# Optimization experiments

Hardware: AMD Instinct MI355X
Metric: run time of the kernel (lower is better)

Reference implementation:

```python
import jax, jax.numpy as jnp
import numpy as np
import math

N = 40000
E = 1280000
HID = 128
NF = 128
NG = 50
L = 3
CUTOFF = 10.0


def ssp(x):
    # shifted softplus: softplus(x) - log(2)
    return jax.nn.softplus(x) - jnp.float32(math.log(2.0))


def setup_inputs() -> dict:
    key = jax.random.key(0)
    ks = jax.random.split(key, 16)
    z = jax.random.randint(ks[0], (N,), 0, 100)
    pos = jax.random.normal(ks[1], (N, 3), dtype=jnp.float32) * 3.0
    batch = jnp.zeros((N,), dtype=jnp.int32)
    edge_index = jax.random.randint(ks[2], (2, E), 0, N)
    s = 0.1
    emb = jax.random.normal(ks[3], (100, HID), dtype=jnp.float32) * s
    mlp_w1 = jax.random.normal(ks[4], (L, NG, NF), dtype=jnp.float32) * s
    mlp_b1 = jnp.zeros((L, NF), dtype=jnp.float32)
    mlp_w2 = jax.random.normal(ks[5], (L, NF, NF), dtype=jnp.float32) * s
    mlp_b2 = jnp.zeros((L, NF), dtype=jnp.float32)
    conv_w1 = jax.random.normal(ks[6], (L, HID, NF), dtype=jnp.float32) * s  # no bias
    conv_w2 = jax.random.normal(ks[7], (L, NF, HID), dtype=jnp.float32) * s
    conv_b2 = jnp.zeros((L, HID), dtype=jnp.float32)
    lin_w = jax.random.normal(ks[8], (L, HID, HID), dtype=jnp.float32) * s
    lin_b = jnp.zeros((L, HID), dtype=jnp.float32)
    lin1_w = jax.random.normal(ks[9], (HID, HID // 2), dtype=jnp.float32) * s
    lin1_b = jnp.zeros((HID // 2,), dtype=jnp.float32)
    return {
        "z": z, "pos": pos, "batch": batch, "edge_index": edge_index,
        "emb": emb, "mlp_w1": mlp_w1, "mlp_b1": mlp_b1, "mlp_w2": mlp_w2,
        "mlp_b2": mlp_b2, "conv_w1": conv_w1, "conv_w2": conv_w2,
        "conv_b2": conv_b2, "lin_w": lin_w, "lin_b": lin_b,
        "lin1_w": lin1_w, "lin1_b": lin1_b,
    }


def reference(z, pos, batch, edge_index, emb, mlp_w1, mlp_b1, mlp_w2, mlp_b2,
              conv_w1, conv_w2, conv_b2, lin_w, lin_b, lin1_w, lin1_b):
    n = z.shape[0]
    row, col = edge_index[0], edge_index[1]
    # edge distances (radius-graph edge weights)
    diff = pos[row] - pos[col]                       # [E,3]
    edge_weight = jnp.sqrt(jnp.sum(diff * diff, axis=-1))  # [E]
    # Gaussian smearing
    offset = jnp.linspace(0.0, CUTOFF, NG, dtype=jnp.float32)
    coeff = -0.5 / (offset[1] - offset[0]) ** 2
    edge_attr = jnp.exp(coeff * (edge_weight[:, None] - offset[None, :]) ** 2)  # [E,NG]
    # cosine cutoff
    C = 0.5 * (jnp.cos(edge_weight * (jnp.pi / CUTOFF)) + 1.0)  # [E]

    h = emb[z]  # [N,HID]
    for l in range(L):
        W = ssp(edge_attr @ mlp_w1[l] + mlp_b1[l]) @ mlp_w2[l] + mlp_b2[l]  # [E,NF]
        W = W * C[:, None]
        x = h @ conv_w1[l]                      # [N,NF]
        msg = x[row] * W                        # gather + filter, [E,NF]
        agg = jax.ops.segment_sum(msg, col, num_segments=n)  # scatter-add, [N,NF]
        x = agg @ conv_w2[l] + conv_b2[l]       # [N,HID]
        x = ssp(x)
        x = x @ lin_w[l] + lin_b[l]
        h = h + x
    return ssp(h @ lin1_w + lin1_b)  # [N,HID//2]
```

## Files before the change

### kernel.cpp

```cpp
#include <hip/hip_runtime.h>
#include <math.h>


typedef _Float16 f16;
typedef _Float16 half8 __attribute__((ext_vector_type(8)));
typedef _Float16 half4v __attribute__((ext_vector_type(4)));
typedef float f32x4 __attribute__((ext_vector_type(4)));

#define NGAUSS 50
#define HIDF   128
#define NBINS  8192
#define DMAXF  40.0f
#define NLAYER 3
#define XST    132
#define BSHIFT 9
#define MAXBUCK 128
#define SCAP  20480

static __device__ __forceinline__ float sspf(float v) {
    return fmaxf(v, 0.0f) + log1pf(expf(-fabsf(v))) - 0.6931471805599453f;
}

__global__ __launch_bounds__(256) void k_stage(const int* __restrict__ ei,
                                               const float* __restrict__ pos,
                                               int* __restrict__ scnt,
                                               uint2* __restrict__ staging,
                                               int E, int nbuck) {
    const float SCALE = (float)(NBINS - 1) / DMAXF;
    __shared__ int bhist[MAXBUCK];
    __shared__ int boff[MAXBUCK];
    __shared__ int gpos[MAXBUCK];
    __shared__ uint2 recs[4096];
    __shared__ unsigned char lbuck[4096];
    int t = threadIdx.x;
    for (int i = t; i < nbuck; i += 256) bhist[i] = 0;
    __syncthreads();
    int e0 = blockIdx.x * 4096;
    int cnt_here = min(4096, E - e0);
    unsigned pay[16];
    unsigned short cc[16];
    short rk[16];
#pragma unroll
    for (int k = 0; k < 16; ++k) {
        int idx = t + k * 256;
        rk[k] = -1;
        if (idx < cnt_here) {
            int e = e0 + idx;
            int r = ei[e], c = ei[E + e];
            float dx = pos[3*r+0] - pos[3*c+0];
            float dy = pos[3*r+1] - pos[3*c+1];
            float dz = pos[3*r+2] - pos[3*c+2];
            float d = sqrtf(dx*dx + dy*dy + dz*dz);
            int ib = (int)(d * SCALE + 0.5f);
            ib = min(ib, NBINS - 1);
            pay[k] = ((unsigned)ib << 16) | (unsigned)r;
            cc[k] = (unsigned short)c;
            rk[k] = (short)atomicAdd(&bhist[c >> BSHIFT], 1);
        }
    }
    __syncthreads();
    if (t == 0) {
        int run = 0;
        for (int b = 0; b < nbuck; ++b) { boff[b] = run; run += bhist[b]; }
    }
    __syncthreads();
    if (t < nbuck) gpos[t] = atomicAdd(&scnt[t], bhist[t]);
    __syncthreads();
#pragma unroll
    for (int k = 0; k < 16; ++k) {
        if (rk[k] >= 0) {
            int b = cc[k] >> BSHIFT;
            int slot = boff[b] + rk[k];
            recs[slot] = make_uint2(pay[k], (unsigned)cc[k]);
            lbuck[slot] = (unsigned char)b;
        }
    }
    __syncthreads();
    for (int i = t; i < cnt_here; i += 256) {
        int b = lbuck[i];
        staging[(size_t)b * SCAP + gpos[b] + (i - boff[b])] = recs[i];
    }
}

__global__ __launch_bounds__(1024) void k_place(const uint2* __restrict__ staging,
                                                const int* __restrict__ scnt,
                                                int* __restrict__ meta,
                                                int* __restrict__ offs,
                                                int n, int nbuck) {
    __shared__ int lcnt[512], loff[512], lcur[512];
    __shared__ int ldsm[SCAP];
    __shared__ int ebase_s;
    int b = blockIdx.x, t = threadIdx.x;
    int cntb = scnt[b];
    if (t == 0) {
        int run = 0;
        for (int j = 0; j < b; ++j) run += scnt[j];
        ebase_s = run;
    }
    for (int j = t; j < 512; j += 1024) { lcnt[j] = 0; lcur[j] = 0; }
    __syncthreads();
    int ebase = ebase_s;
    const uint2* sb = staging + (size_t)b * SCAP;
    for (int i = t; i < cntb; i += 1024)
        atomicAdd(&lcnt[sb[i].y & 511], 1);
    __syncthreads();
    if (t < 512) loff[t] = lcnt[t];
    __syncthreads();
    for (int o = 1; o < 512; o <<= 1) {
        int v = 0;
        if (t < 512) { v = loff[t]; if (t >= o) v += loff[t - o]; }
        __syncthreads();
        if (t < 512) loff[t] = v;
        __syncthreads();
    }
    int nb0 = b << BSHIFT;
    if (t < 512) {
        int node = nb0 + t;
        if (node < n) offs[node] = ebase + loff[t] - lcnt[t];
    }
    if (b == nbuck - 1 && t == 0) offs[n] = ebase + cntb;
    __syncthreads();
    for (int i = t; i < cntb; i += 1024) {
        uint2 r = sb[i];
        int cl = (int)(r.y & 511);
        int lpos = (loff[cl] - lcnt[cl]) + atomicAdd(&lcur[cl], 1);
        if (lpos < SCAP) ldsm[lpos] = (int)r.x;
        else meta[ebase + lpos] = (int)r.x;
    }
    __syncthreads();
    int lim = min(cntb, SCAP);
    for (int i = t; i < lim; i += 1024) meta[ebase + i] = ldsm[i];
}

__global__ __launch_bounds__(128) void k_table(const float* __restrict__ w1,
                                               const float* __restrict__ b1,
                                               const float* __restrict__ w2,
                                               const float* __restrict__ b2,
                                               f16* __restrict__ T) {
    const float DELTA = 10.0f / 49.0f;
    const float COEFF = -0.5f / (DELTA * DELTA);
    const float HSTEP = DMAXF / (float)(NBINS - 1);
    __shared__ float ea[8][NGAUSS];
    __shared__ float u[8][HIDF];
    int l = blockIdx.y, b0 = blockIdx.x * 8, j = threadIdx.x;
    for (int idx = j; idx < 8 * NGAUSS; idx += 128) {
        int bb = idx / NGAUSS, g = idx % NGAUSS;
        float d = (float)(b0 + bb) * HSTEP;
        float diff = d - (float)g * DELTA;
        ea[bb][g] = expf(COEFF * diff * diff);
    }
    __syncthreads();
    float acc[8];
    {
        float bias = b1[l * HIDF + j];
#pragma unroll
        for (int b = 0; b < 8; ++b) acc[b] = bias;
        const float* w1l = w1 + (size_t)l * NGAUSS * HIDF;
        for (int g = 0; g < NGAUSS; ++g) {
            float wv = w1l[g * HIDF + j];
#pragma unroll
            for (int b = 0; b < 8; ++b) acc[b] = fmaf(ea[b][g], wv, acc[b]);
        }
#pragma unroll
        for (int b = 0; b < 8; ++b) u[b][j] = sspf(acc[b]);
    }
    __syncthreads();
    {
        float bias = b2[l * HIDF + j];
#pragma unroll
        for (int b = 0; b < 8; ++b) acc[b] = bias;
        const float* w2l = w2 + (size_t)l * HIDF * HIDF;
        for (int k = 0; k < HIDF; ++k) {
            float wv = w2l[k * HIDF + j];
#pragma unroll
            for (int b = 0; b < 8; ++b) acc[b] = fmaf(u[b][k], wv, acc[b]);
        }
    }
    f16* Tl = T + ((size_t)l * NBINS + b0) * HIDF;
#pragma unroll
    for (int b = 0; b < 8; ++b) {
        float d = (float)(b0 + b) * HSTEP;
        float C = 0.5f * (cosf(d * (float)(M_PI / 10.0)) + 1.0f);
        Tl[b * HIDF + j] = (f16)(acc[b] * C);
    }
}

__global__ void k_wpack(const float* __restrict__ cw1, const float* __restrict__ cw2,
                        const float* __restrict__ lw, const float* __restrict__ l1w,
                        f16* __restrict__ Wp) {
    int mat = blockIdx.y;
    int N = (mat == 9) ? 64 : HIDF;
    int ntiles = N >> 4;
    int tid = blockIdx.x * 256 + threadIdx.x;
    int lane = tid & 63, ks = (tid >> 6) & 3, nt = tid >> 8;
    if (nt >= ntiles) return;
    const float* W;
    if (mat < 9) {
        int l = mat / 3, kind = mat % 3;
        W = (kind == 0 ? cw1 : kind == 1 ? cw2 : lw) + (size_t)l * HIDF * HIDF;
    } else {
        W = l1w;
    }
    int kbase = ks * 32 + (lane >> 4) * 8;
    int col = nt * 16 + (lane & 15);
    half8 st;
#pragma unroll
    for (int j = 0; j < 8; ++j) st[j] = (f16)W[(size_t)(kbase + j) * N + col];
    *(half8*)&Wp[(size_t)mat * 16384 + ((size_t)(nt * 4 + ks) * 64 + lane) * 8] = st;
}

__global__ __launch_bounds__(256) void k_agg(const f16* __restrict__ x,
                                             const f16* __restrict__ T,
                                             const int* __restrict__ meta,
                                             const int* __restrict__ offs,
                                             f16* __restrict__ agg, int n) {
    int node = (blockIdx.x * blockDim.x + threadIdx.x) >> 4;
    int lane = threadIdx.x & 15;
    if (node >= n) return;
    int beg = offs[node], end = offs[node + 1];
    const f16* xj = x + lane * 8;
    const f16* Tj = T + lane * 8;
    float a[8] = {};
    for (int chunk = beg; chunk < end; chunk += 16) {
        int cnt = min(16, end - chunk);
        int mm = meta[chunk + min(lane, cnt - 1)];
        int q = 0;
        for (; q + 8 <= cnt; q += 8) {
            half8 xv[8], tv[8];
#pragma unroll
            for (int k = 0; k < 8; ++k) {
                int y = __shfl(mm, q + k, 16);
                xv[k] = *(const half8*)&xj[(size_t)(y & 0xFFFF) * HIDF];
                tv[k] = *(const half8*)&Tj[(size_t)((unsigned)y >> 16) * HIDF];
            }
#pragma unroll
            for (int k = 0; k < 8; ++k)
#pragma unroll
                for (int j = 0; j < 8; ++j)
                    a[j] = fmaf((float)xv[k][j], (float)tv[k][j], a[j]);
        }
        for (; q < cnt; ++q) {
            int y = __shfl(mm, q, 16);
            half8 xv = *(const half8*)&xj[(size_t)(y & 0xFFFF) * HIDF];
            half8 tv = *(const half8*)&Tj[(size_t)((unsigned)y >> 16) * HIDF];
#pragma unroll
            for (int j = 0; j < 8; ++j)
                a[j] = fmaf((float)xv[j], (float)tv[j], a[j]);
        }
    }
    half8 st;
#pragma unroll
    for (int j = 0; j < 8; ++j) st[j] = (f16)a[j];
    *(half8*)&agg[(size_t)node * HIDF + lane * 8] = st;
}

__global__ __launch_bounds__(256) void k_init_gemm(const int* __restrict__ z,
                                                   const float* __restrict__ emb,
                                                   const f16* __restrict__ w1p,
                                                   f16* __restrict__ xout) {
    int lane = threadIdx.x & 63;
    int wid = threadIdx.x >> 6;
    int m0 = blockIdx.x * 64 + wid * 16;
    int mrow = lane & 15, quad = lane >> 4;
    const float* er = emb + (size_t)z[m0 + mrow] * HIDF + quad * 8;
    half8 afr[4];
#pragma unroll
    for (int ks = 0; ks < 4; ++ks) {
        float4 a = *(const float4*)(er + ks * 32);
        float4 b = *(const float4*)(er + ks * 32 + 4);
        half8 f = {(f16)a.x, (f16)a.y, (f16)a.z, (f16)a.w,
                   (f16)b.x, (f16)b.y, (f16)b.z, (f16)b.w};
        afr[ks] = f;
    }
    f32x4 acc[8];
#pragma unroll
    for (int t = 0; t < 8; ++t) acc[t] = (f32x4){0.f, 0.f, 0.f, 0.f};
    const f16* bp = w1p + (size_t)lane * 8;
#pragma unroll
    for (int t = 0; t < 8; ++t)
#pragma unroll
        for (int ks = 0; ks < 4; ++ks) {
            half8 bfr = *(const half8*)(bp + (size_t)(t * 4 + ks) * 512);
            acc[t] = __builtin_amdgcn_mfma_f32_16x16x32_f16(afr[ks], bfr, acc[t], 0, 0, 0);
        }
    int col0 = lane & 15;
    int growb = m0 + quad * 4;
#pragma unroll
    for (int t = 0; t < 8; ++t)
#pragma unroll
        for (int r = 0; r < 4; ++r)
            xout[(size_t)(growb + r) * HIDF + t * 16 + col0] = (f16)acc[t][r];
}

template <int NT3, bool LAYER0, bool WRITE_H>
__global__ __launch_bounds__(256) void k_fused(const f16* __restrict__ agg,
                                               const f16* __restrict__ w2p,
                                               const float* __restrict__ b2,
                                               const f16* __restrict__ lwp,
                                               const float* __restrict__ lb,
                                               const f16* __restrict__ b3p,
                                               const float* __restrict__ b3,
                                               float* __restrict__ hio,
                                               const int* __restrict__ z,
                                               const float* __restrict__ emb,
                                               f16* __restrict__ xout,
                                               float* __restrict__ fout) {
    __shared__ f16 Xs[4][16][XST];
    int lane = threadIdx.x & 63;
    int wid = threadIdx.x >> 6;
    int m0 = blockIdx.x * 64 + wid * 16;
    int mrow = lane & 15, quad = lane >> 4;
    int col0 = mrow;
    int growb = m0 + quad * 4;
    f16 (*X)[XST] = Xs[wid];

    half8 afr[4];
    {
        const f16* Ar = agg + (size_t)(m0 + mrow) * HIDF + quad * 8;
#pragma unroll
        for (int ks = 0; ks < 4; ++ks) afr[ks] = *(const half8*)(Ar + ks * 32);
    }
    f32x4 acc[8];
#pragma unroll
    for (int t = 0; t < 8; ++t) acc[t] = (f32x4){0.f, 0.f, 0.f, 0.f};
    {
        const f16* bp = w2p + (size_t)lane * 8;
#pragma unroll
        for (int t = 0; t < 8; ++t)
#pragma unroll
            for (int ks = 0; ks < 4; ++ks) {
                half8 bfr = *(const half8*)(bp + (size_t)(t * 4 + ks) * 512);
                acc[t] = __builtin_amdgcn_mfma_f32_16x16x32_f16(afr[ks], bfr, acc[t], 0, 0, 0);
            }
    }
#pragma unroll
    for (int t = 0; t < 8; ++t) {
        int col = t * 16 + col0;
        float bv = b2[col];
#pragma unroll
        for (int r = 0; r < 4; ++r)
            X[quad * 4 + r][col] = (f16)sspf(acc[t][r] + bv);
    }
#pragma unroll
    for (int ks = 0; ks < 4; ++ks) {
        half4v lo = *(const half4v*)&X[mrow][ks * 32 + quad * 8];
        half4v hi = *(const half4v*)&X[mrow][ks * 32 + quad * 8 + 4];
        half8 f;
#pragma unroll
        for (int j = 0; j < 4; ++j) { f[j] = lo[j]; f[4 + j] = hi[j]; }
        afr[ks] = f;
    }
#pragma unroll
    for (int t = 0; t < 8; ++t) acc[t] = (f32x4){0.f, 0.f, 0.f, 0.f};
    {
        const f16* bp = lwp + (size_t)lane * 8;
#pragma unroll
        for (int t = 0; t < 8; ++t)
#pragma unroll
            for (int ks = 0; ks < 4; ++ks) {
                half8 bfr = *(const half8*)(bp + (size_t)(t * 4 + ks) * 512);
                acc[t] = __builtin_amdgcn_mfma_f32_16x16x32_f16(afr[ks], bfr, acc[t], 0, 0, 0);
            }
    }
    int zr[4];
    if (LAYER0) {
#pragma unroll
        for (int r = 0; r < 4; ++r) zr[r] = z[growb + r];
    }
#pragma unroll
    for (int t = 0; t < 8; ++t) {
        int col = t * 16 + col0;
        float bv = lb[col];
#pragma unroll
        for (int r = 0; r < 4; ++r) {
            int grow = growb + r;
            float resid = LAYER0 ? emb[(size_t)zr[r] * HIDF + col]
                                 : hio[(size_t)grow * HIDF + col];
            float hp = acc[t][r] + bv + resid;
            if (WRITE_H) hio[(size_t)grow * HIDF + col] = hp;
            X[quad * 4 + r][col] = (f16)hp;
        }
    }
#pragma unroll
    for (int ks = 0; ks < 4; ++ks) {
        half4v lo = *(const half4v*)&X[mrow][ks * 32 + quad * 8];
        half4v hi = *(const half4v*)&X[mrow][ks * 32 + quad * 8 + 4];
        half8 f;
#pragma unroll
        for (int j = 0; j < 4; ++j) { f[j] = lo[j]; f[4 + j] = hi[j]; }
        afr[ks] = f;
    }
#pragma unroll
    for (int t = 0; t < NT3; ++t) acc[t] = (f32x4){0.f, 0.f, 0.f, 0.f};
    {
        const f16* bp = b3p + (size_t)lane * 8;
#pragma unroll
        for (int t = 0; t < NT3; ++t)
#pragma unroll
            for (int ks = 0; ks < 4; ++ks) {
                half8 bfr = *(const half8*)(bp + (size_t)(t * 4 + ks) * 512);
                acc[t] = __builtin_amdgcn_mfma_f32_16x16x32_f16(afr[ks], bfr, acc[t], 0, 0, 0);
            }
    }
    if (NT3 == 8) {
#pragma unroll
        for (int t = 0; t < 8; ++t)
#pragma unroll
            for (int r = 0; r < 4; ++r)
                xout[(size_t)(growb + r) * HIDF + t * 16 + col0] = (f16)acc[t][r];
    } else {
#pragma unroll
        for (int t = 0; t < NT3; ++t) {
            int col = t * 16 + col0;
            float bv = b3[col];
#pragma unroll
            for (int r = 0; r < 4; ++r)
                fout[(size_t)(growb + r) * (NT3 * 16) + col] = sspf(acc[t][r] + bv);
        }
    }
}

extern "C" void kernel_launch(void* const* d_in, const int* in_sizes, int n_in,
                              void* d_out, int out_size, void* d_ws, size_t ws_size,
                              hipStream_t stream) {
    const int*   z       = (const int*)d_in[0];
    const float* pos     = (const float*)d_in[1];
    const int*   ei      = (const int*)d_in[3];
    const float* emb     = (const float*)d_in[4];
    const float* mlp_w1  = (const float*)d_in[5];
    const float* mlp_b1  = (const float*)d_in[6];
    const float* mlp_w2  = (const float*)d_in[7];
    const float* mlp_b2  = (const float*)d_in[8];
    const float* conv_w1 = (const float*)d_in[9];
    const float* conv_w2 = (const float*)d_in[10];
    const float* conv_b2 = (const float*)d_in[11];
    const float* lin_w   = (const float*)d_in[12];
    const float* lin_b   = (const float*)d_in[13];
    const float* lin1_w  = (const float*)d_in[14];
    const float* lin1_b  = (const float*)d_in[15];
    float* out = (float*)d_out;

    int n = in_sizes[0];
    int E = in_sizes[3] / 2;
    int nbuck = (n + 511) >> 9;

    char* ws = (char*)d_ws;
    size_t off = 0;
    auto alloc = [&](size_t bytes) -> void* {
        void* p = ws + off;
        off = (off + bytes + 255) & ~(size_t)255;
        return p;
    };
    float* h     = (float*)alloc((size_t)n * HIDF * 4);
    f16*   x16   = (f16*)alloc((size_t)n * HIDF * 2);
    f16*   agg16 = (f16*)alloc((size_t)n * HIDF * 2);
    f16*   T16   = (f16*)alloc((size_t)NLAYER * NBINS * HIDF * 2);
    int*   meta  = (int*)alloc((size_t)E * 4);
    int*   offs  = (int*)alloc((size_t)(n + 1) * 4);
    int*   scnt  = (int*)alloc((size_t)nbuck * 4);
    uint2* staging = (uint2*)alloc((size_t)nbuck * SCAP * 8);
    f16*   Wp    = (f16*)alloc((size_t)10 * 16384 * 2);

    const int tb = 256;
    hipMemsetAsync(scnt, 0, (size_t)nbuck * 4, stream);
    hipLaunchKernelGGL(k_stage, dim3((E + 4095) / 4096), dim3(tb), 0, stream,
                       ei, pos, scnt, staging, E, nbuck);
    hipLaunchKernelGGL(k_place, dim3(nbuck), dim3(1024), 0, stream,
                       staging, scnt, meta, offs, n, nbuck);
    hipLaunchKernelGGL(k_table, dim3(NBINS / 8, NLAYER), dim3(128), 0, stream,
                       mlp_w1, mlp_b1, mlp_w2, mlp_b2, T16);
    hipLaunchKernelGGL(k_wpack, dim3(8, 10), dim3(tb), 0, stream,
                       conv_w1, conv_w2, lin_w, lin1_w, Wp);

    int gemmblocks = n / 64;
    int aggblocks = (n * 16 + tb - 1) / tb;
    hipLaunchKernelGGL(k_init_gemm, dim3(gemmblocks), dim3(tb), 0, stream,
                       z, emb, Wp + (size_t)0 * 16384, x16);
    hipLaunchKernelGGL(k_agg, dim3(aggblocks), dim3(tb), 0, stream,
                       x16, T16 + (size_t)0 * NBINS * HIDF, meta, offs, agg16, n);
    hipLaunchKernelGGL(HIP_KERNEL_NAME(k_fused<8, true, true>), dim3(gemmblocks), dim3(tb), 0, stream,
                       agg16, Wp + (size_t)1 * 16384, conv_b2 + 0 * HIDF,
                       Wp + (size_t)2 * 16384, lin_b + 0 * HIDF,
                       Wp + (size_t)3 * 16384, (const float*)nullptr,
                       h, z, emb, x16, (float*)nullptr);
    hipLaunchKernelGGL(k_agg, dim3(aggblocks), dim3(tb), 0, stream,
                       x16, T16 + (size_t)1 * NBINS * HIDF, meta, offs, agg16, n);
    hipLaunchKernelGGL(HIP_KERNEL_NAME(k_fused<8, false, true>), dim3(gemmblocks), dim3(tb), 0, stream,
                       agg16, Wp + (size_t)4 * 16384, conv_b2 + 1 * HIDF,
                       Wp + (size_t)5 * 16384, lin_b + 1 * HIDF,
                       Wp + (size_t)6 * 16384, (const float*)nullptr,
                       h, (const int*)nullptr, (const float*)nullptr, x16, (float*)nullptr);
    hipLaunchKernelGGL(k_agg, dim3(aggblocks), dim3(tb), 0, stream,
                       x16, T16 + (size_t)2 * NBINS * HIDF, meta, offs, agg16, n);
    hipLaunchKernelGGL(HIP_KERNEL_NAME(k_fused<4, false, false>), dim3(gemmblocks), dim3(tb), 0, stream,
                       agg16, Wp + (size_t)7 * 16384, conv_b2 + 2 * HIDF,
                       Wp + (size_t)8 * 16384, lin_b + 2 * HIDF,
                       Wp + (size_t)9 * 16384, lin1_b,
                       h, (const int*)nullptr, (const float*)nullptr, (f16*)nullptr, out);
    (void)n_in; (void)out_size; (void)ws_size;
}
```

Baseline: 440.7 us.

## Fuse edge aggregation into per-layer fused GEMM kernel with ping-pong x buffers

```diff
diff --git a/kernel.cpp b/kernel.cpp
--- a/kernel.cpp
+++ b/kernel.cpp
@@ -209,51 +209,6 @@
     *(half8*)&Wp[(size_t)mat * 16384 + ((size_t)(nt * 4 + ks) * 64 + lane) * 8] = st;
 }
 
-__global__ __launch_bounds__(256) void k_agg(const f16* __restrict__ x,
-                                             const f16* __restrict__ T,
-                                             const int* __restrict__ meta,
-                                             const int* __restrict__ offs,
-                                             f16* __restrict__ agg, int n) {
-    int node = (blockIdx.x * blockDim.x + threadIdx.x) >> 4;
-    int lane = threadIdx.x & 15;
-    if (node >= n) return;
-    int beg = offs[node], end = offs[node + 1];
-    const f16* xj = x + lane * 8;
-    const f16* Tj = T + lane * 8;
-    float a[8] = {};
-    for (int chunk = beg; chunk < end; chunk += 16) {
-        int cnt = min(16, end - chunk);
-        int mm = meta[chunk + min(lane, cnt - 1)];
-        int q = 0;
-        for (; q + 8 <= cnt; q += 8) {
-            half8 xv[8], tv[8];
-#pragma unroll
-            for (int k = 0; k < 8; ++k) {
-                int y = __shfl(mm, q + k, 16);
-                xv[k] = *(const half8*)&xj[(size_t)(y & 0xFFFF) * HIDF];
-                tv[k] = *(const half8*)&Tj[(size_t)((unsigned)y >> 16) * HIDF];
-            }
-#pragma unroll
-            for (int k = 0; k < 8; ++k)
-#pragma unroll
-                for (int j = 0; j < 8; ++j)
-                    a[j] = fmaf((float)xv[k][j], (float)tv[k][j], a[j]);
-        }
-        for (; q < cnt; ++q) {
-            int y = __shfl(mm, q, 16);
-            half8 xv = *(const half8*)&xj[(size_t)(y & 0xFFFF) * HIDF];
-            half8 tv = *(const half8*)&Tj[(size_t)((unsigned)y >> 16) * HIDF];
-#pragma unroll
-            for (int j = 0; j < 8; ++j)
-                a[j] = fmaf((float)xv[j], (float)tv[j], a[j]);
-        }
-    }
-    half8 st;
-#pragma unroll
-    for (int j = 0; j < 8; ++j) st[j] = (f16)a[j];
-    *(half8*)&agg[(size_t)node * HIDF + lane * 8] = st;
-}
-
 __global__ __launch_bounds__(256) void k_init_gemm(const int* __restrict__ z,
                                                    const float* __restrict__ emb,
                                                    const f16* __restrict__ w1p,
@@ -293,7 +248,10 @@
 }
 
 template <int NT3, bool LAYER0, bool WRITE_H>
-__global__ __launch_bounds__(256) void k_fused(const f16* __restrict__ agg,
+__global__ __launch_bounds__(256) void k_fused(const f16* __restrict__ x,
+                                               const f16* __restrict__ T,
+                                               const int* __restrict__ meta,
+                                               const int* __restrict__ offs,
                                                const f16* __restrict__ w2p,
                                                const float* __restrict__ b2,
                                                const f16* __restrict__ lwp,
@@ -305,6 +263,7 @@
                                                const float* __restrict__ emb,
                                                f16* __restrict__ xout,
                                                float* __restrict__ fout) {
+    __shared__ f16 Ags[4][16][XST];
     __shared__ f16 Xs[4][16][XST];
     int lane = threadIdx.x & 63;
     int wid = threadIdx.x >> 6;
@@ -312,13 +271,61 @@
     int mrow = lane & 15, quad = lane >> 4;
     int col0 = mrow;
     int growb = m0 + quad * 4;
+    f16 (*Ag)[XST] = Ags[wid];
     f16 (*X)[XST] = Xs[wid];
 
+    {
+        const f16* xj = x + mrow * 8;
+        const f16* Tj = T + mrow * 8;
+        for (int s = 0; s < 4; ++s) {
+            int node = m0 + quad * 4 + s;
+            int beg = offs[node], end = offs[node + 1];
+            float a[8] = {};
+            for (int chunk = beg; chunk < end; chunk += 16) {
+                int cnt = min(16, end - chunk);
+                int mm = meta[chunk + min(mrow, cnt - 1)];
+                int q = 0;
+                for (; q + 8 <= cnt; q += 8) {
+                    half8 xv[8], tv[8];
+#pragma unroll
+                    for (int k = 0; k < 8; ++k) {
+                        int y = __shfl(mm, q + k, 16);
+                        xv[k] = *(const half8*)&xj[(size_t)(y & 0xFFFF) * HIDF];
+                        tv[k] = *(const half8*)&Tj[(size_t)((unsigned)y >> 16) * HIDF];
+                    }
+#pragma unroll
+                    for (int k = 0; k < 8; ++k)
+#pragma unroll
+                        for (int j = 0; j < 8; ++j)
+                            a[j] = fmaf((float)xv[k][j], (float)tv[k][j], a[j]);
+                }
+                for (; q < cnt; ++q) {
+                    int y = __shfl(mm, q, 16);
+                    half8 xv = *(const half8*)&xj[(size_t)(y & 0xFFFF) * HIDF];
+                    half8 tv = *(const half8*)&Tj[(size_t)((unsigned)y >> 16) * HIDF];
+#pragma unroll
+                    for (int j = 0; j < 8; ++j)
+                        a[j] = fmaf((float)xv[j], (float)tv[j], a[j]);
+                }
+            }
+            int r = quad * 4 + s;
+            half4v lo, hi;
+#pragma unroll
+            for (int j = 0; j < 4; ++j) { lo[j] = (f16)a[j]; hi[j] = (f16)a[4 + j]; }
+            *(half4v*)&Ag[r][mrow * 8] = lo;
+            *(half4v*)&Ag[r][mrow * 8 + 4] = hi;
+        }
+    }
+
     half8 afr[4];
-    {
-        const f16* Ar = agg + (size_t)(m0 + mrow) * HIDF + quad * 8;
-#pragma unroll
-        for (int ks = 0; ks < 4; ++ks) afr[ks] = *(const half8*)(Ar + ks * 32);
+#pragma unroll
+    for (int ks = 0; ks < 4; ++ks) {
+        half4v lo = *(const half4v*)&Ag[mrow][ks * 32 + quad * 8];
+        half4v hi = *(const half4v*)&Ag[mrow][ks * 32 + quad * 8 + 4];
+        half8 f;
+#pragma unroll
+        for (int j = 0; j < 4; ++j) { f[j] = lo[j]; f[4 + j] = hi[j]; }
+        afr[ks] = f;
     }
     f32x4 acc[8];
 #pragma unroll
@@ -452,8 +459,8 @@
         return p;
     };
     float* h     = (float*)alloc((size_t)n * HIDF * 4);
-    f16*   x16   = (f16*)alloc((size_t)n * HIDF * 2);
-    f16*   agg16 = (f16*)alloc((size_t)n * HIDF * 2);
+    f16*   x16a  = (f16*)alloc((size_t)n * HIDF * 2);
+    f16*   x16b  = (f16*)alloc((size_t)n * HIDF * 2);
     f16*   T16   = (f16*)alloc((size_t)NLAYER * NBINS * HIDF * 2);
     int*   meta  = (int*)alloc((size_t)E * 4);
     int*   offs  = (int*)alloc((size_t)(n + 1) * 4);
@@ -473,27 +480,23 @@
                        conv_w1, conv_w2, lin_w, lin1_w, Wp);
 
     int gemmblocks = n / 64;
-    int aggblocks = (n * 16 + tb - 1) / tb;
     hipLaunchKernelGGL(k_init_gemm, dim3(gemmblocks), dim3(tb), 0, stream,
-                       z, emb, Wp + (size_t)0 * 16384, x16);
-    hipLaunchKernelGGL(k_agg, dim3(aggblocks), dim3(tb), 0, stream,
-                       x16, T16 + (size_t)0 * NBINS * HIDF, meta, offs, agg16, n);
+                       z, emb, Wp + (size_t)0 * 16384, x16a);
     hipLaunchKernelGGL(HIP_KERNEL_NAME(k_fused<8, true, true>), dim3(gemmblocks), dim3(tb), 0, stream,
-                       agg16, Wp + (size_t)1 * 16384, conv_b2 + 0 * HIDF,
+                       x16a, T16 + (size_t)0 * NBINS * HIDF, meta, offs,
+                       Wp + (size_t)1 * 16384, conv_b2 + 0 * HIDF,
                        Wp + (size_t)2 * 16384, lin_b + 0 * HIDF,
                        Wp + (size_t)3 * 16384, (const float*)nullptr,
-                       h, z, emb, x16, (float*)nullptr);
-    hipLaunchKernelGGL(k_agg, dim3(aggblocks), dim3(tb), 0, stream,
-                       x16, T16 + (size_t)1 * NBINS * HIDF, meta, offs, agg16, n);
+                       h, z, emb, x16b, (float*)nullptr);
     hipLaunchKernelGGL(HIP_KERNEL_NAME(k_fused<8, false, true>), dim3(gemmblocks), dim3(tb), 0, stream,
-                       agg16, Wp + (size_t)4 * 16384, conv_b2 + 1 * HIDF,
+                       x16b, T16 + (size_t)1 * NBINS * HIDF, meta, offs,
+                       Wp + (size_t)4 * 16384, conv_b2 + 1 * HIDF,
                        Wp + (size_t)5 * 16384, lin_b + 1 * HIDF,
                        Wp + (size_t)6 * 16384, (const float*)nullptr,
-                       h, (const int*)nullptr, (const float*)nullptr, x16, (float*)nullptr);
-    hipLaunchKernelGGL(k_agg, dim3(aggblocks), dim3(tb), 0, stream,
-                       x16, T16 + (size_t)2 * NBINS * HIDF, meta, offs, agg16, n);
+                       h, (const int*)nullptr, (const float*)nullptr, x16a, (float*)nullptr);
     hipLaunchKernelGGL(HIP_KERNEL_NAME(k_fused<4, false, false>), dim3(gemmblocks), dim3(tb), 0, stream,
-                       agg16, Wp + (size_t)7 * 16384, conv_b2 + 2 * HIDF,
+                       x16a, T16 + (size_t)2 * NBINS * HIDF, meta, offs,
+                       Wp + (size_t)7 * 16384, conv_b2 + 2 * HIDF,
                        Wp + (size_t)8 * 16384, lin_b + 2 * HIDF,
                        Wp + (size_t)9 * 16384, lin1_b,
                        h, (const int*)nullptr, (const float*)nullptr, (f16*)nullptr, out);
```

Result: slower. 493.8 us (+12.1%).
